# Optimization experiments

Measured on AMD Instinct MI355X. Metric: run time of the kernel, lower is better.

Reference implementation:

```python
import jax, jax.numpy as jnp
import numpy as np

D_MODEL = 1024
NUM_HEAD = 16
HEAD_DIM = 64
FFN = 4096
EPS = 1e-5


def setup_inputs() -> dict:
    key = jax.random.key(0)
    ks = jax.random.split(key, 8)
    B, S, D = 2, 2048, D_MODEL
    s = 0.02
    return {
        "x": jax.random.normal(ks[0], (B, S, D), dtype=jnp.float32),
        "mask": jnp.zeros((S, S), dtype=jnp.float32),
        "Wqkv": jax.random.normal(ks[1], (D, 3 * D), dtype=jnp.float32) * s,
        "bqkv": jnp.zeros((3 * D,), dtype=jnp.float32),
        "Wo": jax.random.normal(ks[2], (D, D), dtype=jnp.float32) * s,
        "bo": jnp.zeros((D,), dtype=jnp.float32),
        "gamma": jnp.ones((D,), dtype=jnp.float32),
        "beta": jnp.zeros((D,), dtype=jnp.float32),
        "W1": jax.random.normal(ks[3], (D, FFN), dtype=jnp.float32) * s,
        "b1": jnp.zeros((FFN,), dtype=jnp.float32),
        "W2": jax.random.normal(ks[4], (FFN, D), dtype=jnp.float32) * s,
        "b2": jnp.zeros((D,), dtype=jnp.float32),
    }


def reference(x, mask, Wqkv, bqkv, Wo, bo, gamma, beta, W1, b1, W2, b2):
    B, S, D = x.shape
    H, hd = NUM_HEAD, HEAD_DIM

    def layernorm(v):
        m = v.mean(axis=-1, keepdims=True)
        var = ((v - m) ** 2).mean(axis=-1, keepdims=True)
        return gamma * (v - m) / jnp.sqrt(var + EPS) + beta

    # --- multihead attention ---
    qkv = (x @ Wqkv + bqkv).reshape(B, S, H, 3, hd).transpose(0, 2, 1, 3, 4)  # [B,H,S,3,hd]
    q, k, v = qkv[..., 0, :], qkv[..., 1, :], qkv[..., 2, :]
    scores = jnp.einsum("bhqd,bhkd->bhqk", q, k) / jnp.sqrt(jnp.float32(hd))
    scores = scores + mask  # [S,S] broadcasts over [B,H,S,S]
    attn = jax.nn.softmax(scores, axis=-1)
    vals = jnp.einsum("bhqk,bhkd->bhqd", attn, v)
    attn_out = vals.transpose(0, 2, 1, 3).reshape(B, S, D) @ Wo + bo

    # residual + (shared) layernorm
    x2 = layernorm(x + attn_out)

    # --- feedforward ---
    ff = jax.nn.relu(x2 @ W1 + b1) @ W2 + b2
    return layernorm(x2 + ff)
```

## Files before the change

### kernel.cpp

```cpp
#include <hip/hip_runtime.h>
#include <hip/hip_bf16.h>
#include <stdint.h>


typedef __bf16 bf16;
typedef bf16  bf16x8 __attribute__((ext_vector_type(8)));
typedef bf16  bf16x4 __attribute__((ext_vector_type(4)));
typedef float f32x4  __attribute__((ext_vector_type(4)));
typedef unsigned int u32x4 __attribute__((ext_vector_type(4)));

#define MFMA16(a,b,c) __builtin_amdgcn_mfma_f32_16x16x32_bf16(a,b,c,0,0,0)

#if __has_builtin(__builtin_amdgcn_exp2f)
#define EXP2F(x) __builtin_amdgcn_exp2f(x)
#else
#define EXP2F(x) exp2f(x)
#endif

static __device__ __forceinline__ void lds_cp16(const bf16* g, bf16* l) {
  __builtin_amdgcn_global_load_lds(
      (const __attribute__((address_space(1))) void*)g,
      (__attribute__((address_space(3))) void*)l, 16, 0, 0);
}

__global__ __launch_bounds__(256) void cast_bf16(const float* __restrict__ in,
                                                 bf16* __restrict__ out, int n4) {
  const int stride = gridDim.x * 256;
  for (int i = blockIdx.x * 256 + threadIdx.x; i < n4; i += stride) {
    f32x4 v = *(const f32x4*)(in + (size_t)i * 4);
    bf16x4 o; o[0]=(bf16)v[0]; o[1]=(bf16)v[1]; o[2]=(bf16)v[2]; o[3]=(bf16)v[3];
    *(bf16x4*)(out + (size_t)i * 4) = o;
  }
}

__global__ __launch_bounds__(256) void transpose_cast(const float* __restrict__ W,
                                                      bf16* __restrict__ Wt,
                                                      int K, int N) {
  __shared__ float t[32][33];
  const int n0 = blockIdx.x * 32, k0 = blockIdx.y * 32;
  const int tid = threadIdx.x;
  const int r = tid >> 3, c4 = (tid & 7) * 4;
  f32x4 v = *(const f32x4*)&W[(size_t)(k0 + r) * N + n0 + c4];
  t[r][c4+0] = v[0]; t[r][c4+1] = v[1]; t[r][c4+2] = v[2]; t[r][c4+3] = v[3];
  __syncthreads();
  bf16x4 o;
  o[0]=(bf16)t[c4+0][r]; o[1]=(bf16)t[c4+1][r]; o[2]=(bf16)t[c4+2][r]; o[3]=(bf16)t[c4+3][r];
  *(bf16x4*)&Wt[(size_t)(n0 + r) * K + k0 + c4] = o;
}

template <int EPI, int BN, int KSPLIT>
__global__ __launch_bounds__(256) void gemm_bf16(
    const bf16* __restrict__ A, const bf16* __restrict__ Bt,
    int M, int N, int K,
    const float* __restrict__ bias,
    float* __restrict__ outf0, float* __restrict__ outf1,
    bf16* __restrict__ outb,
    bf16* __restrict__ qb, bf16* __restrict__ kb, bf16* __restrict__ vb) {
  const int tid = threadIdx.x;
  const int w = tid >> 6, lane = tid & 63;
  const int l15 = lane & 15, lhi = lane >> 4;
  const int wr = w >> 1, wc = w & 1;
  constexpr int NI = BN / 32;
  const int nbm = M >> 7, nbn = N / BN;
  const int nwg = nbm * nbn * KSPLIT;
  const int bid = (blockIdx.x & 7) * (nwg >> 3) + (blockIdx.x >> 3);
  const int ks = bid / (nbm * nbn);
  const int r2 = bid % (nbm * nbn);
  const int bm = r2 % nbm;
  const int bn = r2 / nbm;
  const int kbeg = ks * (K / KSPLIT);

  __shared__ alignas(16) bf16 Al[128 * 32];
  __shared__ alignas(16) bf16 Bl[BN * 32];

  f32x4 acc[4][NI];
#pragma unroll
  for (int i = 0; i < 4; i++)
#pragma unroll
    for (int j = 0; j < NI; j++) acc[i][j] = (f32x4){0.f, 0.f, 0.f, 0.f};

  const int swz = ((tid & 3) ^ ((tid >> 2) & 3)) * 8;
  const bf16* ap = A + (size_t)(bm * 128 + (tid >> 2)) * K + kbeg + swz;
  const bf16* bp = Bt + (size_t)(bn * BN + (tid >> 2)) * K + kbeg + swz;
  const size_t rstep = (size_t)64 * K;
  bf16* la0 = &Al[w * 512]; bf16* la1 = &Al[2048 + w * 512];
  bf16* lb0 = &Bl[w * 512];
  bf16* lb1 = (BN == 128) ? &Bl[2048 + w * 512] : nullptr;

  const int rs0 = (lhi ^ (l15 & 3)) * 8;

  const int nk = K / (32 * KSPLIT);
  for (int kt = 0; kt < nk; ++kt) {
    lds_cp16(ap, la0);
    lds_cp16(ap + rstep, la1);
    lds_cp16(bp, lb0);
    if constexpr (BN == 128) lds_cp16(bp + rstep, lb1);
    ap += 32; bp += 32;
    __syncthreads();
    bf16x8 af[4], bfv[NI];
#pragma unroll
    for (int mi = 0; mi < 4; mi++)
      af[mi] = *(const bf16x8*)&Al[(wr * 64 + mi * 16 + l15) * 32 + rs0];
#pragma unroll
    for (int ni = 0; ni < NI; ni++)
      bfv[ni] = *(const bf16x8*)&Bl[(wc * (BN / 2) + ni * 16 + l15) * 32 + rs0];
#pragma unroll
    for (int mi = 0; mi < 4; mi++)
#pragma unroll
      for (int ni = 0; ni < NI; ni++)
        acc[mi][ni] = MFMA16(af[mi], bfv[ni], acc[mi][ni]);
    __syncthreads();
  }

  const int row0 = bm * 128 + wr * 64 + lhi * 4;
  const int col0 = bn * BN + wc * (BN / 2) + l15;
#pragma unroll
  for (int ni = 0; ni < NI; ni++) {
    const int c = col0 + ni * 16;
    if (EPI == 0) {
      const float bc = bias[c];
      const int h = c / 192;
      const int rem = c - h * 192;
      const int wq = rem >> 6, d = rem & 63;
#pragma unroll
      for (int mi = 0; mi < 4; mi++)
#pragma unroll
        for (int j = 0; j < 4; j++) {
          const int m = row0 + mi * 16 + j;
          const int b = m >> 11, s = m & 2047;
          const float val = acc[mi][ni][j] + bc;
          const size_t base = (size_t)(b * 16 + h) * (2048 * 64);
          if (wq == 0)      qb[base + (size_t)s * 64 + d] = (bf16)val;
          else if (wq == 1) kb[base + (size_t)s * 64 + d] = (bf16)val;
          else              vb[base + (size_t)d * 2048 + s] = (bf16)val;
        }
    } else if (EPI == 2) {
      const float bc = bias[c];
#pragma unroll
      for (int mi = 0; mi < 4; mi++)
#pragma unroll
        for (int j = 0; j < 4; j++) {
          const int m = row0 + mi * 16 + j;
          outb[(size_t)m * N + c] = (bf16)fmaxf(acc[mi][ni][j] + bc, 0.f);
        }
    } else {
      float* po = ks ? outf1 : outf0;
#pragma unroll
      for (int mi = 0; mi < 4; mi++)
#pragma unroll
        for (int j = 0; j < 4; j++) {
          const int m = row0 + mi * 16 + j;
          po[(size_t)m * N + c] = acc[mi][ni][j];
        }
    }
  }
}

__global__ __launch_bounds__(256) void attn_fwd(const bf16* __restrict__ qg,
                                                const bf16* __restrict__ kg,
                                                const bf16* __restrict__ vg,
                                                bf16* __restrict__ og) {
  const int bid = (blockIdx.x & 7) * 64 + (blockIdx.x >> 3);
  const int bh = bid >> 4;
  const int qp = bid & 15;
  const int tid = threadIdx.x, w = tid >> 6, lane = tid & 63;
  const int l15 = lane & 15, lhi = lane >> 4;

  __shared__ alignas(16) bf16 Kl[2][64 * 64];
  __shared__ alignas(16) bf16 Vl[2][64 * 64];
  __shared__ alignas(16) bf16 PlA[4][16 * 64];
  __shared__ alignas(16) bf16 PlB[4][16 * 64];

  const size_t bho = (size_t)bh * (2048 * 64);
  const int q0 = qp * 128 + w * 16;

  bf16x8 qfA0, qfA1, qfB0, qfB1;
  {
    const float qs = 0.125f * 1.44269504f;
    const bf16* qpA = qg + bho + (size_t)(q0 + l15) * 64 + lhi * 8;
    qfA0 = *(const bf16x8*)qpA;
    qfA1 = *(const bf16x8*)(qpA + 32);
    const bf16* qpB = qpA + 64 * 64;
    qfB0 = *(const bf16x8*)qpB;
    qfB1 = *(const bf16x8*)(qpB + 32);
#pragma unroll
    for (int i = 0; i < 8; i++) {
      qfA0[i] = (bf16)((float)qfA0[i] * qs);
      qfA1[i] = (bf16)((float)qfA1[i] * qs);
      qfB0[i] = (bf16)((float)qfB0[i] * qs);
      qfB1[i] = (bf16)((float)qfB1[i] * qs);
    }
  }

  bf16x8 ones;
#pragma unroll
  for (int i = 0; i < 8; i++) ones[i] = (bf16)1.0f;

  const int x7 = l15 & 7;
  const int slot0 = (lhi ^ x7) * 8;
  const int slot1 = ((lhi + 4) ^ x7) * 8;
  int rowb[4];
#pragma unroll
  for (int nt = 0; nt < 4; nt++) rowb[nt] = (l15 + 16 * nt) * 64;

  const int r0 = w * 8 + (lane >> 3);
  const int sx = ((lane & 7) ^ ((lane >> 3) & 7)) * 8;
  const bf16* kbase = kg + bho + (size_t)r0 * 64 + sx;
  const bf16* vbase = vg + bho + (size_t)r0 * 2048 + sx;
  bf16* klds = &Kl[0][0] + w * 512;
  bf16* vlds = &Vl[0][0] + w * 512;

#define STAGE(kt, buf)                                                        \
  do {                                                                        \
    const int bo = (buf) * 4096;                                              \
    lds_cp16(kbase + (kt) * 4096,           klds + bo);                       \
    lds_cp16(kbase + (kt) * 4096 + 2048,    klds + bo + 2048);                \
    lds_cp16(vbase + (kt) * 64,             vlds + bo);                       \
    lds_cp16(vbase + (kt) * 64 + 32 * 2048, vlds + bo + 2048);                \
  } while (0)

  f32x4 accvA[4], accvB[4];
#pragma unroll
  for (int nt = 0; nt < 4; nt++) {
    accvA[nt] = (f32x4){0.f, 0.f, 0.f, 0.f};
    accvB[nt] = (f32x4){0.f, 0.f, 0.f, 0.f};
  }
  f32x4 accsA = (f32x4){0.f, 0.f, 0.f, 0.f};
  f32x4 accsB = (f32x4){0.f, 0.f, 0.f, 0.f};
  const f32x4 zero = (f32x4){0.f, 0.f, 0.f, 0.f};

  STAGE(0, 0);
  __syncthreads();

  for (int kt = 0; kt < 32; ++kt) {
    const int buf = kt & 1;
    if (kt < 31) STAGE(kt + 1, buf ^ 1);
    const bf16* kb_ = &Kl[buf][0];
    const bf16* vb_ = &Vl[buf][0];

    f32x4 scA[4], scB[4];
    __builtin_amdgcn_s_setprio(1);
#pragma unroll
    for (int nt = 0; nt < 4; nt++) {
      bf16x8 kf0 = *(const bf16x8*)&kb_[rowb[nt] + slot0];
      bf16x8 kf1 = *(const bf16x8*)&kb_[rowb[nt] + slot1];
      scA[nt] = MFMA16(qfA1, kf1, MFMA16(qfA0, kf0, zero));
      scB[nt] = MFMA16(qfB1, kf1, MFMA16(qfB0, kf0, zero));
    }
    __builtin_amdgcn_s_setprio(0);

#pragma unroll
    for (int nt = 0; nt < 4; nt++)
#pragma unroll
      for (int r = 0; r < 4; r++) {
        const int q = lhi * 4 + r;
        const int col = (l15 + 16 * nt) ^ ((q & 7) << 3);
        PlA[w][q * 64 + col] = (bf16)EXP2F(scA[nt][r]);
        PlB[w][q * 64 + col] = (bf16)EXP2F(scB[nt][r]);
      }

    bf16x8 pfA0 = *(const bf16x8*)&PlA[w][l15 * 64 + slot0];
    bf16x8 pfA1 = *(const bf16x8*)&PlA[w][l15 * 64 + slot1];
    bf16x8 pfB0 = *(const bf16x8*)&PlB[w][l15 * 64 + slot0];
    bf16x8 pfB1 = *(const bf16x8*)&PlB[w][l15 * 64 + slot1];
    __builtin_amdgcn_s_setprio(1);
#pragma unroll
    for (int nt = 0; nt < 4; nt++) {
      bf16x8 vf0 = *(const bf16x8*)&vb_[rowb[nt] + slot0];
      bf16x8 vf1 = *(const bf16x8*)&vb_[rowb[nt] + slot1];
      accvA[nt] = MFMA16(pfA1, vf1, MFMA16(pfA0, vf0, accvA[nt]));
      accvB[nt] = MFMA16(pfB1, vf1, MFMA16(pfB0, vf0, accvB[nt]));
    }
    accsA = MFMA16(pfA1, ones, MFMA16(pfA0, ones, accsA));
    accsB = MFMA16(pfB1, ones, MFMA16(pfB0, ones, accsB));
    __builtin_amdgcn_s_setprio(0);
    __syncthreads();
  }
#undef STAGE

  const int b = bh >> 4, h = bh & 15;
  f32x4 invA, invB;
#pragma unroll
  for (int r = 0; r < 4; r++) { invA[r] = 1.f / accsA[r]; invB[r] = 1.f / accsB[r]; }
#pragma unroll
  for (int nt = 0; nt < 4; nt++)
#pragma unroll
    for (int r = 0; r < 4; r++) {
      const int qrow = q0 + lhi * 4 + r;
      og[(size_t)(b * 2048 + qrow) * 1024 + h * 64 + nt * 16 + l15] =
          (bf16)(accvA[nt][r] * invA[r]);
      og[(size_t)(b * 2048 + qrow + 64) * 1024 + h * 64 + nt * 16 + l15] =
          (bf16)(accvB[nt][r] * invB[r]);
    }
}

template <int WB>
__global__ __launch_bounds__(256) void reduce_ln(
    const float* __restrict__ p0, const float* __restrict__ p1,
    const float* __restrict__ bias, const float* __restrict__ resid,
    const float* __restrict__ gamma, const float* __restrict__ beta,
    float* __restrict__ outf, bf16* __restrict__ outb) {
  const int row = blockIdx.x;
  const int tid = threadIdx.x;
  const size_t off = (size_t)row * 1024 + tid * 4;
  f32x4 a = *(const f32x4*)(p0 + off);
  f32x4 b = *(const f32x4*)(p1 + off);
  f32x4 rr = *(const f32x4*)(resid + off);
  f32x4 bs = *(const f32x4*)(bias + tid * 4);
  f32x4 v;
#pragma unroll
  for (int i = 0; i < 4; i++) v[i] = a[i] + b[i] + rr[i] + bs[i];
  float s = v[0] + v[1] + v[2] + v[3];
  float ss = v[0]*v[0] + v[1]*v[1] + v[2]*v[2] + v[3]*v[3];
#pragma unroll
  for (int m = 1; m < 64; m <<= 1) { s += __shfl_xor(s, m); ss += __shfl_xor(ss, m); }
  __shared__ float red[8];
  const int w = tid >> 6;
  if ((tid & 63) == 0) { red[w * 2] = s; red[w * 2 + 1] = ss; }
  __syncthreads();
  s = red[0] + red[2] + red[4] + red[6];
  ss = red[1] + red[3] + red[5] + red[7];
  const float mean = s * (1.f / 1024.f);
  const float rstd = rsqrtf(ss * (1.f / 1024.f) - mean * mean + 1e-5f);
  f32x4 g = *(const f32x4*)(gamma + tid * 4);
  f32x4 bb = *(const f32x4*)(beta + tid * 4);
  f32x4 o;
#pragma unroll
  for (int i = 0; i < 4; i++) o[i] = g[i] * (v[i] - mean) * rstd + bb[i];
  *(f32x4*)(outf + off) = o;
  if (WB) {
    bf16x4 ob;
#pragma unroll
    for (int i = 0; i < 4; i++) ob[i] = (bf16)o[i];
    *(bf16x4*)(outb + off) = ob;
  }
}

extern "C" void kernel_launch(void* const* d_in, const int* in_sizes, int n_in,
                              void* d_out, int out_size, void* d_ws, size_t ws_size,
                              hipStream_t stream) {
  (void)in_sizes; (void)n_in; (void)out_size;
  const float* x     = (const float*)d_in[0];
  const float* Wqkv  = (const float*)d_in[2];
  const float* bqkv  = (const float*)d_in[3];
  const float* Wo    = (const float*)d_in[4];
  const float* bo    = (const float*)d_in[5];
  const float* gamma = (const float*)d_in[6];
  const float* beta  = (const float*)d_in[7];
  const float* W1    = (const float*)d_in[8];
  const float* b1    = (const float*)d_in[9];
  const float* W2    = (const float*)d_in[10];
  const float* b2    = (const float*)d_in[11];
  float* out = (float*)d_out;

  if (ws_size < 100663296) return;
  char* ws = (char*)d_ws;
  bf16* xb    = (bf16*)(ws + 0);
  bf16* Wqkvt = (bf16*)(ws + 8388608);
  bf16* Wot   = (bf16*)(ws + 14680064);
  bf16* W1t   = (bf16*)(ws + 16777216);
  bf16* W2t   = (bf16*)(ws + 25165824);
  bf16* qb    = (bf16*)(ws + 33554432);
  bf16* kb    = (bf16*)(ws + 41943040);
  bf16* vb    = (bf16*)(ws + 50331648);
  float* wo_p0 = (float*)(ws + 33554432);
  float* wo_p1 = (float*)(ws + 50331648);
  float* x2f  = (float*)(ws + 75497472);
  bf16* x2b   = (bf16*)(ws + 92274688);
  bf16* ff1   = (bf16*)(ws + 33554432);
  float* f2_p1 = (float*)(ws + 0);
  float* f2_p0 = out;
  bf16* vals  = xb;

  cast_bf16<<<2048, 256, 0, stream>>>(x, xb, 4096 * 1024 / 4);
  transpose_cast<<<dim3(96, 32), 256, 0, stream>>>(Wqkv, Wqkvt, 1024, 3072);
  transpose_cast<<<dim3(32, 32), 256, 0, stream>>>(Wo, Wot, 1024, 1024);
  transpose_cast<<<dim3(128, 32), 256, 0, stream>>>(W1, W1t, 1024, 4096);
  transpose_cast<<<dim3(32, 128), 256, 0, stream>>>(W2, W2t, 4096, 1024);

  gemm_bf16<0, 128, 1><<<768, 256, 0, stream>>>(xb, Wqkvt, 4096, 3072, 1024,
      bqkv, nullptr, nullptr, nullptr, qb, kb, vb);
  attn_fwd<<<512, 256, 0, stream>>>(qb, kb, vb, vals);
  gemm_bf16<4, 64, 2><<<1024, 256, 0, stream>>>(vals, Wot, 4096, 1024, 1024,
      nullptr, wo_p0, wo_p1, nullptr, nullptr, nullptr, nullptr);
  reduce_ln<1><<<4096, 256, 0, stream>>>(wo_p0, wo_p1, bo, x, gamma, beta, x2f, x2b);
  gemm_bf16<2, 128, 1><<<1024, 256, 0, stream>>>(x2b, W1t, 4096, 4096, 1024,
      b1, nullptr, nullptr, ff1, nullptr, nullptr, nullptr);
  gemm_bf16<4, 64, 2><<<1024, 256, 0, stream>>>(ff1, W2t, 4096, 1024, 4096,
      nullptr, f2_p0, f2_p1, nullptr, nullptr, nullptr, nullptr);
  reduce_ln<0><<<4096, 256, 0, stream>>>(f2_p0, f2_p1, b2, x2f, gamma, beta, out, nullptr);
}
```

Measured before the change: 286.9 us.

## Double-buffer GEMM LDS tiles and raise wave priority around MFMA block

Splits the GEMM's shared-memory A and B tiles into two buffers so the global-to-LDS copy for the next K slice is issued while the current slice is being read and multiplied. This drops one of the two block barriers per iteration and hides load latency behind MFMA work. It also raises wave priority during the MFMA burst with s_setprio. The cost is doubled LDS use per block, which may lower occupancy. Correctness relies on the single remaining barrier also covering completion of the asynchronous global_load_lds into the other buffer.

```diff
diff --git a/kernel.cpp b/kernel.cpp
--- a/kernel.cpp
+++ b/kernel.cpp
@@ -70,8 +70,8 @@
   const int bn = r2 / nbm;
   const int kbeg = ks * (K / KSPLIT);
 
-  __shared__ alignas(16) bf16 Al[128 * 32];
-  __shared__ alignas(16) bf16 Bl[BN * 32];
+  __shared__ alignas(16) bf16 Al[2][128 * 32];
+  __shared__ alignas(16) bf16 Bl[2][BN * 32];
 
   f32x4 acc[4][NI];
 #pragma unroll
@@ -83,34 +83,41 @@
   const bf16* ap = A + (size_t)(bm * 128 + (tid >> 2)) * K + kbeg + swz;
   const bf16* bp = Bt + (size_t)(bn * BN + (tid >> 2)) * K + kbeg + swz;
   const size_t rstep = (size_t)64 * K;
-  bf16* la0 = &Al[w * 512]; bf16* la1 = &Al[2048 + w * 512];
-  bf16* lb0 = &Bl[w * 512];
-  bf16* lb1 = (BN == 128) ? &Bl[2048 + w * 512] : nullptr;
+
+#define GSTAGE(kt, buf)                                                       \
+  do {                                                                        \
+    lds_cp16(ap + (kt) * 32,         &Al[buf][w * 512]);                      \
+    lds_cp16(ap + (kt) * 32 + rstep, &Al[buf][2048 + w * 512]);               \
+    lds_cp16(bp + (kt) * 32,         &Bl[buf][w * 512]);                      \
+    if constexpr (BN == 128)                                                  \
+      lds_cp16(bp + (kt) * 32 + rstep, &Bl[buf][2048 + w * 512]);             \
+  } while (0)
 
   const int rs0 = (lhi ^ (l15 & 3)) * 8;
 
   const int nk = K / (32 * KSPLIT);
+  GSTAGE(0, 0);
+  __syncthreads();
   for (int kt = 0; kt < nk; ++kt) {
-    lds_cp16(ap, la0);
-    lds_cp16(ap + rstep, la1);
-    lds_cp16(bp, lb0);
-    if constexpr (BN == 128) lds_cp16(bp + rstep, lb1);
-    ap += 32; bp += 32;
-    __syncthreads();
+    const int buf = kt & 1;
+    if (kt + 1 < nk) GSTAGE(kt + 1, buf ^ 1);
     bf16x8 af[4], bfv[NI];
 #pragma unroll
     for (int mi = 0; mi < 4; mi++)
-      af[mi] = *(const bf16x8*)&Al[(wr * 64 + mi * 16 + l15) * 32 + rs0];
+      af[mi] = *(const bf16x8*)&Al[buf][(wr * 64 + mi * 16 + l15) * 32 + rs0];
 #pragma unroll
     for (int ni = 0; ni < NI; ni++)
-      bfv[ni] = *(const bf16x8*)&Bl[(wc * (BN / 2) + ni * 16 + l15) * 32 + rs0];
+      bfv[ni] = *(const bf16x8*)&Bl[buf][(wc * (BN / 2) + ni * 16 + l15) * 32 + rs0];
+    __builtin_amdgcn_s_setprio(1);
 #pragma unroll
     for (int mi = 0; mi < 4; mi++)
 #pragma unroll
       for (int ni = 0; ni < NI; ni++)
         acc[mi][ni] = MFMA16(af[mi], bfv[ni], acc[mi][ni]);
+    __builtin_amdgcn_s_setprio(0);
     __syncthreads();
   }
+#undef GSTAGE
 
   const int row0 = bm * 128 + wr * 64 + lhi * 4;
   const int col0 = bn * BN + wc * (BN / 2) + l15;
```

Measured after the change: 263.8 us. -8.1%, faster.
